# Kernel tuning notes

Measured on AMD Instinct MI355X. Metric: run time of the kernel, lower is better.

The kernel has to match this reference:

```python
import jax, jax.numpy as jnp
import numpy as np

POS_IDX = np.array([0, 2, 4, 10, 14, 20, 22, 24])   # +w taps on 5x5 ring
NEG_IDX = np.array([6, 7, 8, 11, 13, 16, 17, 18])   # -w taps on inner 3x3 ring (center stays 0)


def setup_inputs() -> dict:
    key = jax.random.key(0)
    kx, kw = jax.random.split(key)
    x = jax.random.normal(kx, (16, 256, 128, 128), dtype=jnp.float32)
    weight = jax.random.normal(kw, (256, 1, 3, 3), dtype=jnp.float32) * 0.1
    return {"x": x, "weight": weight}


def _build_rpdc_kernel(weight):
    # weight: [C, 1, 3, 3] -> sparse 5x5 kernel [C, 1, 5, 5]
    C = weight.shape[0]
    w = weight.reshape(C, 1, 9)
    tap = w[:, :, 1:]  # taps 1..8 (skip w[0]); center of 5x5 is forced to 0
    buf = jnp.zeros((C, 1, 25), dtype=weight.dtype)
    buf = buf.at[:, :, POS_IDX].set(tap)
    buf = buf.at[:, :, NEG_IDX].set(-tap)
    return buf.reshape(C, 1, 5, 5)


def reference(x, weight):
    # Depthwise conv (groups = in_channels), dilation=1 -> padding = 2 (same conv)
    C = weight.shape[0]
    kernel = _build_rpdc_kernel(weight)
    return jax.lax.conv_general_dilated(
        x, kernel,
        window_strides=(1, 1),
        padding=[(2, 2), (2, 2)],
        rhs_dilation=(1, 1),
        dimension_numbers=("NCHW", "OIHW", "NCHW"),
        feature_group_count=C,
    )
```

## Files before the change

### kernel.cpp

```cpp
#include <hip/hip_runtime.h>


#define HH 128
#define WW 128
#define CHUNK 32
#define SPB 8

__global__ __launch_bounds__(256, 4) void rpdc_kernel(
    const float* __restrict__ x, const float* __restrict__ wt,
    float* __restrict__ out, int C)
{
    const int tid   = threadIdx.x;
    const int l     = tid & 31;
    const int s     = blockIdx.x * SPB + (tid >> 5);
    const int plane = s >> 2;
    const int h0    = (s & 3) * CHUNK;
    const int c     = plane & (C - 1);

    const float* wp = wt + (size_t)c * 9;
    const float t0 = wp[1], t1 = wp[2], t2 = wp[3], t3 = wp[4];
    const float t4 = wp[5], t5 = wp[6], t6 = wp[7], t7 = wp[8];

    const int w0  = l * 4;
    const int olp = (l == 0) ? 0 : (w0 - 2);
    const int orp = (l == 31) ? (w0 + 2) : (w0 + 4);
    const float ml = (l == 0) ? 0.f : 1.f;
    const float mr = (l == 31) ? 0.f : 1.f;

    const float* xb = x + (size_t)plane * (HH * WW) + (size_t)h0 * WW;
    float* ob = out + (size_t)plane * (HH * WW) + (size_t)h0 * WW + w0;

    float ring[6][8];
    float2 tl, tr; float4 tv;

    auto issue = [&](int rr, float2& a, float4& v, float2& b) {
        const int r = h0 + rr;
        if ((unsigned)r < (unsigned)HH) {
            const float* p = xb + rr * WW;
            a = *(const float2*)(p + olp);
            v = *(const float4*)(p + w0);
            b = *(const float2*)(p + orp);
        } else {
            a = make_float2(0.f, 0.f);
            v = make_float4(0.f, 0.f, 0.f, 0.f);
            b = make_float2(0.f, 0.f);
        }
    };
    auto insert = [&](float (&row)[8], const float2& a, const float4& v,
                      const float2& b) {
        row[0] = a.x * ml; row[1] = a.y * ml;
        row[2] = v.x; row[3] = v.y; row[4] = v.z; row[5] = v.w;
        row[6] = b.x * mr; row[7] = b.y * mr;
    };

#pragma unroll
    for (int k = 0; k < 5; ++k) {
        float2 a, b; float4 v;
        issue(k - 2, a, v, b);
        insert(ring[k], a, v, b);
    }
    issue(3, tl, tv, tr);

#pragma unroll
    for (int h = 0; h < CHUNK; ++h) {
        float2 nl, nr; float4 nv;
        issue(h < CHUNK - 2 ? h + 4 : HH, nl, nv, nr);

        insert(ring[(h + 5) % 6], tl, tv, tr);

        const float (&A)[8]  = ring[h % 6];
        const float (&B)[8]  = ring[(h + 1) % 6];
        const float (&Cc)[8] = ring[(h + 2) % 6];
        const float (&D)[8]  = ring[(h + 3) % 6];
        const float (&E)[8]  = ring[(h + 4) % 6];

        float o[4];
#pragma unroll
        for (int j = 0; j < 4; ++j) {
            float r = t0 * (A[j]     - B[j + 1]);
            r      += t1 * (A[j + 2] - B[j + 2]);
            r      += t2 * (A[j + 4] - B[j + 3]);
            r      += t3 * (Cc[j]     - Cc[j + 1]);
            r      += t4 * (Cc[j + 4] - Cc[j + 3]);
            r      += t5 * (E[j]     - D[j + 1]);
            r      += t6 * (E[j + 2] - D[j + 2]);
            r      += t7 * (E[j + 4] - D[j + 3]);
            o[j] = r;
        }
        *(float4*)(ob + h * WW) = make_float4(o[0], o[1], o[2], o[3]);

        tl = nl; tv = nv; tr = nr;
    }
}

extern "C" void kernel_launch(void* const* d_in, const int* in_sizes, int n_in,
                              void* d_out, int out_size, void* d_ws, size_t ws_size,
                              hipStream_t stream) {
    const float* x = (const float*)d_in[0];
    const float* wt = (const float*)d_in[1];
    float* out = (float*)d_out;

    const int C = in_sizes[1] / 9;
    const int planes = in_sizes[0] / (HH * WW);

    dim3 grid(planes * (HH / CHUNK) / SPB);
    dim3 block(256);
    rpdc_kernel<<<grid, block, 0, stream>>>(x, wt, out, C);
}
```

Baseline: 438.9 us.

## Fetch row halos via ds_bpermute instead of extra global loads

Each lane now loads only its own float4 per row and gets the two-column left and right halos from neighbouring lanes with ds_bpermute, removing the two float2 global loads per row. The prefetch depth goes from one row ahead to two, and launch bounds are raised to 5 waves per SIMD. Permutes use a 64-lane wave address, so lanes 31/32 exchange across the two row-segments, but the ml/mr masks zero those edges. This trades global memory traffic for LDS permute instructions and slightly higher register pressure from the deeper prefetch.

```diff
diff --git a/kernel.cpp b/kernel.cpp
--- a/kernel.cpp
+++ b/kernel.cpp
@@ -6,7 +6,11 @@
 #define CHUNK 32
 #define SPB 8
 
-__global__ __launch_bounds__(256, 4) void rpdc_kernel(
+__device__ __forceinline__ float bperm(int addr, float v) {
+    return __int_as_float(__builtin_amdgcn_ds_bpermute(addr, __float_as_int(v)));
+}
+
+__global__ __launch_bounds__(256, 5) void rpdc_kernel(
     const float* __restrict__ x, const float* __restrict__ wt,
     float* __restrict__ out, int C)
 {
@@ -21,52 +25,52 @@
     const float t0 = wp[1], t1 = wp[2], t2 = wp[3], t3 = wp[4];
     const float t4 = wp[5], t5 = wp[6], t6 = wp[7], t7 = wp[8];
 
-    const int w0  = l * 4;
-    const int olp = (l == 0) ? 0 : (w0 - 2);
-    const int orp = (l == 31) ? (w0 + 2) : (w0 + 4);
+    const int w0 = l * 4;
     const float ml = (l == 0) ? 0.f : 1.f;
     const float mr = (l == 31) ? 0.f : 1.f;
 
-    const float* xb = x + (size_t)plane * (HH * WW) + (size_t)h0 * WW;
+    const int lane = tid & 63;
+    const int upA  = ((lane - 1) & 63) * 4;
+    const int dnA  = ((lane + 1) & 63) * 4;
+
+    const float* xb = x + (size_t)plane * (HH * WW) + (size_t)h0 * WW + w0;
     float* ob = out + (size_t)plane * (HH * WW) + (size_t)h0 * WW + w0;
 
     float ring[6][8];
-    float2 tl, tr; float4 tv;
+    float4 s0, s1;
 
-    auto issue = [&](int rr, float2& a, float4& v, float2& b) {
+    auto issue = [&](int rr, float4& v) {
         const int r = h0 + rr;
         if ((unsigned)r < (unsigned)HH) {
-            const float* p = xb + rr * WW;
-            a = *(const float2*)(p + olp);
-            v = *(const float4*)(p + w0);
-            b = *(const float2*)(p + orp);
+            v = *(const float4*)(xb + rr * WW);
         } else {
-            a = make_float2(0.f, 0.f);
             v = make_float4(0.f, 0.f, 0.f, 0.f);
-            b = make_float2(0.f, 0.f);
         }
     };
-    auto insert = [&](float (&row)[8], const float2& a, const float4& v,
-                      const float2& b) {
-        row[0] = a.x * ml; row[1] = a.y * ml;
+    auto insert = [&](float (&row)[8], const float4& v) {
+        row[0] = bperm(upA, v.z) * ml;
+        row[1] = bperm(upA, v.w) * ml;
         row[2] = v.x; row[3] = v.y; row[4] = v.z; row[5] = v.w;
-        row[6] = b.x * mr; row[7] = b.y * mr;
+        row[6] = bperm(dnA, v.x) * mr;
+        row[7] = bperm(dnA, v.y) * mr;
     };
 
 #pragma unroll
     for (int k = 0; k < 5; ++k) {
-        float2 a, b; float4 v;
-        issue(k - 2, a, v, b);
-        insert(ring[k], a, v, b);
+        float4 v;
+        issue(k - 2, v);
+        insert(ring[k], v);
     }
-    issue(3, tl, tv, tr);
+    issue(3, s0);
+    issue(4, s1);
 
 #pragma unroll
     for (int h = 0; h < CHUNK; ++h) {
-        float2 nl, nr; float4 nv;
-        issue(h < CHUNK - 2 ? h + 4 : HH, nl, nv, nr);
+        float4 nv;
+        issue((h <= CHUNK - 4) ? (h + 5) : HH, nv);
 
-        insert(ring[(h + 5) % 6], tl, tv, tr);
+        insert(ring[(h + 5) % 6], s0);
+        s0 = s1; s1 = nv;
 
         const float (&A)[8]  = ring[h % 6];
         const float (&B)[8]  = ring[(h + 1) % 6];
@@ -88,8 +92,6 @@
             o[j] = r;
         }
         *(float4*)(ob + h * WW) = make_float4(o[0], o[1], o[2], o[3]);
-
-        tl = nl; tv = nv; tr = nr;
     }
 }
 
```

After: 658.7 us. 1.5x slower.
